# Performance work log

Hardware: AMD Instinct MI355X
Metric: run time of the kernel (lower is better)

Reference implementation:

```python
import jax, jax.numpy as jnp
from jax import lax
import numpy as np

D_IN = 512    # inputdim
HID = 128     # hiddendim
D_INNER = 2 * HID   # 256
D_PROJ = 2 * D_INNER  # 512
N_STATE = 16
R_DT = 8      # ceil(128/16)
B, H, W = 8, 32, 32


def _layernorm(y, g, b):
    mu = y.mean(-1, keepdims=True)
    var = ((y - mu) ** 2).mean(-1, keepdims=True)
    return (y - mu) / jnp.sqrt(var + 1e-5) * g + b


def _ssm(x, xw, dtw, dtb, Al, Dv, g, be):
    # x: [B, D, L] -> y: [B, L, D]  (Mamba selective scan, delta_softplus=True)
    Bb, D, L = x.shape
    n = Al.shape[1]
    xd = jnp.einsum('bdl,kd->blk', x, xw)             # [B,L,R+2N]
    dts = xd[..., :R_DT]
    Bs = xd[..., R_DT:R_DT + n]                        # [B,L,N]
    Cs = xd[..., R_DT + n:]                            # [B,L,N]
    delta = jax.nn.softplus(jnp.einsum('blr,dr->bld', dts, dtw) + dtb)  # [B,L,D]
    A = -jnp.exp(Al)                                   # [D,N]
    xt = x.transpose(0, 2, 1)                          # [B,L,D]
    dA = jnp.exp(delta[..., None] * A)                 # [B,L,D,N]
    dBx = delta[..., None] * Bs[:, :, None, :] * xt[..., None]  # [B,L,D,N]

    def step(h, inp):
        da, dbx, c = inp
        h = h * da + dbx
        return h, jnp.einsum('bdn,bn->bd', h, c)

    h0 = jnp.zeros((Bb, D, n), x.dtype)
    _, ys = lax.scan(step, h0, (dA.transpose(1, 0, 2, 3),
                                dBx.transpose(1, 0, 2, 3),
                                Cs.transpose(1, 0, 2)))
    y = ys.transpose(1, 0, 2) + xt * Dv                # [B,L,D]
    return _layernorm(y, g, be)


def _up2(y, h, w):
    Bb, L, C = y.shape
    img = y.transpose(0, 2, 1).reshape(Bb, C, h, w)
    img = jnp.repeat(jnp.repeat(img, 2, axis=2), 2, axis=3)
    return img.reshape(Bb, C, 4 * L).transpose(0, 2, 1)


def _conv1x1(x, w, b):
    return jnp.einsum('bchw,oc->bohw', x, w) + b[None, :, None, None]


def _conv2s2(x, w, b):
    out = lax.conv_general_dilated(x, w, (2, 2), 'VALID',
                                   dimension_numbers=('NCHW', 'OIHW', 'NCHW'))
    return out + b[None, :, None, None]


def _forward(input_f, in_w, in_b, c1_w, c1_b, c2_w, c2_b, c3_w, c3_b, out_w, out_b,
             xw1, dtw1, dtb1, Al1, Dv1, g1, be1,
             xw2, dtw2, dtb2, Al2, Dv2, g2, be2,
             xw3, dtw3, dtb3, Al3, Dv3, g3, be3):
    xz = _conv1x1(input_f, in_w, in_b)
    x, z = jnp.split(xz, 2, axis=1)
    f1 = _conv1x1(x, c1_w, c1_b)                      # [B,256,H,W]
    f2 = _conv2s2(f1, c2_w, c2_b)                     # [B,256,H/2,W/2]
    f3 = _conv2s2(f2, c3_w, c3_b)                     # [B,256,H/4,W/4]

    Bb, C, h3, w3 = f3.shape
    fx3 = f3.reshape(Bb, C, h3 * w3)
    y3 = _ssm(fx3, xw3, dtw3, dtb3, Al3, Dv3, g3, be3) + \
         jnp.flip(_ssm(jnp.flip(fx3, -1), xw3, dtw3, dtb3, Al3, Dv3, g3, be3), 1)
    y2_ = _up2(y3, h3, w3)

    _, _, h2, w2 = f2.shape
    fx2 = f2.reshape(Bb, C, h2 * w2)
    y2 = _ssm(fx2, xw2, dtw2, dtb2, Al2, Dv2, g2, be2) + \
         jnp.flip(_ssm(jnp.flip(fx2, -1), xw2, dtw2, dtb2, Al2, Dv2, g2, be2), 1) + y2_
    y1_ = _up2(y2, h2, w2)

    _, _, h1, w1 = f1.shape
    fx1 = f1.reshape(Bb, C, h1 * w1)
    # NOTE: source uses fssm1 forward and fssm2 on the flipped sequence
    y1 = _ssm(fx1, xw1, dtw1, dtb1, Al1, Dv1, g1, be1) + \
         jnp.flip(_ssm(jnp.flip(fx1, -1), xw2, dtw2, dtb2, Al2, Dv2, g2, be2), 1) + y1_

    out1 = y1.transpose(0, 2, 1).reshape(Bb, C, h1, w1)
    out = out1 * jax.nn.silu(z)
    return _conv1x1(out, out_w, out_b)


def setup_inputs() -> dict:
    key = jax.random.key(0)
    ks = iter(jax.random.split(key, 64))
    def nrm(shape, s=0.05):
        return (jax.random.normal(next(ks), shape, dtype=jnp.float32) * s)
    inp = {
        'input_f': jax.random.normal(next(ks), (B, D_IN, H, W), dtype=jnp.float32),
        'in_w': nrm((D_PROJ, D_IN)), 'in_b': nrm((D_PROJ,)),
        'c1_w': nrm((D_INNER, D_INNER)), 'c1_b': nrm((D_INNER,)),
        'c2_w': nrm((D_INNER, D_INNER, 2, 2)), 'c2_b': nrm((D_INNER,)),
        'c3_w': nrm((D_INNER, D_INNER, 2, 2)), 'c3_b': nrm((D_INNER,)),
        'out_w': nrm((D_IN, D_INNER)), 'out_b': nrm((D_IN,)),
    }
    Al = jnp.log(jnp.tile(jnp.arange(1, N_STATE + 1, dtype=jnp.float32), (D_INNER, 1)))
    for i in (1, 2, 3):
        inp[f'xw{i}'] = nrm((R_DT + 2 * N_STATE, D_INNER))
        inp[f'dtw{i}'] = nrm((D_INNER, R_DT), s=R_DT ** -0.5)
        inp[f'dtb{i}'] = nrm((D_INNER,)) - 4.0   # inv-softplus of small dt
        inp[f'Al{i}'] = Al
        inp[f'Dv{i}'] = jnp.ones((D_INNER,), jnp.float32)
        inp[f'g{i}'] = jnp.ones((D_INNER,), jnp.float32)
        inp[f'be{i}'] = jnp.zeros((D_INNER,), jnp.float32)
    return inp


def reference(input_f, in_w, in_b, c1_w, c1_b, c2_w, c2_b, c3_w, c3_b, out_w, out_b,
              xw1, dtw1, dtb1, Al1, Dv1, g1, be1,
              xw2, dtw2, dtb2, Al2, Dv2, g2, be2,
              xw3, dtw3, dtb3, Al3, Dv3, g3, be3):
    return _forward(input_f, in_w, in_b, c1_w, c1_b, c2_w, c2_b, c3_w, c3_b, out_w, out_b,
                    xw1, dtw1, dtb1, Al1, Dv1, g1, be1,
                    xw2, dtw2, dtb2, Al2, Dv2, g2, be2,
                    xw3, dtw3, dtb3, Al3, Dv3, g3, be3)
```

## Files before the change

### kernel.cpp

```cpp
#include <hip/hip_runtime.h>
#include <cstddef>

#define DEV static __device__ __forceinline__

typedef __attribute__((ext_vector_type(8))) short short8;
typedef __attribute__((ext_vector_type(4))) float floatx4;

DEV float siluf(float v) { return v / (1.f + expf(-v)); }

DEV unsigned short f2bf(float f) {
  unsigned int u = __float_as_uint(f);
  u += 0x7fff + ((u >> 16) & 1);
  return (unsigned short)(u >> 16);
}
DEV float bf2f(unsigned short u) {
  return __uint_as_float(((unsigned int)u) << 16);
}
DEV float4 bf2f4(ushort4 v) {
  return make_float4(bf2f(v.x), bf2f(v.y), bf2f(v.z), bf2f(v.w));
}

template <int CTRL>
DEV float qadd(float v) {
  int s = __builtin_amdgcn_update_dpp(__float_as_int(v), __float_as_int(v),
                                      CTRL, 0xF, 0xF, false);
  return v + __int_as_float(s);
}

__global__ __launch_bounds__(256) void prep_k(
    const float* __restrict__ in_w, const float* __restrict__ c1_w,
    const float* __restrict__ c2_w, const float* __restrict__ c3_w,
    const float* __restrict__ out_w, const float* __restrict__ xw1,
    const float* __restrict__ xw2, const float* __restrict__ xw3,
    unsigned short* __restrict__ wsW,
    const float* __restrict__ input_f, unsigned short* __restrict__ inT)
{
  __shared__ float tile[32][33];
  int bid = blockIdx.x;
  int t = threadIdx.x;
  if (bid < 3960) {
    int gid = bid * 256 + t;
    float v;
    if      (gid < 262144)  v = in_w[gid];
    else if (gid < 327680)  v = c1_w[gid - 262144];
    else if (gid < 589824)  {
      int off = gid - 327680;
      int o = off >> 10, kk = off & 1023, ij = kk >> 8, c = kk & 255;
      v = c2_w[o * 1024 + c * 4 + ij];
    }
    else if (gid < 851968)  {
      int off = gid - 589824;
      int o = off >> 10, kk = off & 1023, ij = kk >> 8, c = kk & 255;
      v = c3_w[o * 1024 + c * 4 + ij];
    }
    else if (gid < 983040)  v = out_w[gid - 851968];
    else if (gid < 993280)  v = xw1[gid - 983040];
    else if (gid < 1003520) v = xw2[gid - 993280];
    else                    v = xw3[gid - 1003520];
    wsW[gid] = f2bf(v);
  } else {
    int idx = bid - 3960;
    int b = idx >> 9, blk = idx & 511;
    int pt = blk & 31, ct = blk >> 5;
    int p0 = pt * 32, c0 = ct * 32;
    int r = t >> 5, cc = t & 31;
#pragma unroll
    for (int i = 0; i < 4; i++) {
      int row = r + 8 * i;
      tile[row][cc] = input_f[((size_t)b * 512 + c0 + row) * 1024 + p0 + cc];
    }
    __syncthreads();
#pragma unroll
    for (int i = 0; i < 4; i++) {
      int row = r + 8 * i;
      inT[((size_t)b * 1024 + p0 + row) * 512 + c0 + cc] = f2bf(tile[cc][row]);
    }
  }
}

template <int EPI>
DEV void mgemm_body(const unsigned short* __restrict__ A, long long sA,
                    const unsigned short* __restrict__ B, long long sB,
                    const float* __restrict__ bias,
                    void* __restrict__ O1, void* __restrict__ O2,
                    int M, int N, int K, int Mt, int Nt, int bid)
{
  __shared__ __align__(16) unsigned short Ab[128 * 40];
  __shared__ __align__(16) unsigned short Bb[128 * 40];
  int tiles = Mt * Nt;
  int bb = bid / tiles;
  int rr = bid - bb * tiles;
  int m0 = (rr / Nt) * 128;
  int n0 = (rr % Nt) * 128;
  const unsigned short* Ap = A + (size_t)bb * sA;
  const unsigned short* Bp = B + (size_t)bb * sB;

  int t = threadIdx.x;
  int lane = t & 63;
  int wm = ((t >> 7) & 1) * 64;
  int wn = ((t >> 6) & 1) * 64;
  int l15 = lane & 15, quad = lane >> 4;

  int srow = t >> 1;
  int shalf = (t & 1) * 16;
  int arow = m0 + srow; if (arow > M - 1) arow = M - 1;
  int brow = n0 + srow; if (brow > N - 1) brow = N - 1;
  const unsigned short* ap = Ap + (size_t)arow * K + shalf;
  const unsigned short* bp = Bp + (size_t)brow * K + shalf;
  unsigned short* as = &Ab[srow * 40 + shalf];
  unsigned short* bs = &Bb[srow * 40 + shalf];

  floatx4 acc[4][4] = {};

  for (int k0 = 0; k0 < K; k0 += 32) {
    uint4 a0 = *(const uint4*)(ap + k0);
    uint4 a1 = *(const uint4*)(ap + k0 + 8);
    uint4 b0 = *(const uint4*)(bp + k0);
    uint4 b1 = *(const uint4*)(bp + k0 + 8);
    __syncthreads();
    *(uint4*)as = a0; *(uint4*)(as + 8) = a1;
    *(uint4*)bs = b0; *(uint4*)(bs + 8) = b1;
    __syncthreads();
    short8 af[4], bf[4];
#pragma unroll
    for (int i = 0; i < 4; i++)
      af[i] = *(const short8*)&Ab[(wm + i * 16 + l15) * 40 + quad * 8];
#pragma unroll
    for (int j = 0; j < 4; j++)
      bf[j] = *(const short8*)&Bb[(wn + j * 16 + l15) * 40 + quad * 8];
#pragma unroll
    for (int i = 0; i < 4; i++)
#pragma unroll
      for (int j = 0; j < 4; j++)
        acc[i][j] = __builtin_amdgcn_mfma_f32_16x16x32_bf16(af[i], bf[j],
                                                            acc[i][j], 0, 0, 0);
  }

  if (EPI == 1) {
    unsigned short* Yt = (unsigned short*)O1;
    unsigned short* Ys = (unsigned short*)O2;
    float bn[4]; int nn[4];
#pragma unroll
    for (int j = 0; j < 4; j++) { nn[j] = n0 + wn + j * 16 + l15; bn[j] = bias[nn[j]]; }
#pragma unroll
    for (int i = 0; i < 4; i++) {
      int pixb = m0 + wm + i * 16 + quad * 4;
#pragma unroll
      for (int j = 0; j < 4; j++) {
        int n = nn[j];
        if (n < 256) {
#pragma unroll
          for (int r = 0; r < 4; r++)
            Yt[((size_t)bb * 1024 + pixb + r) * 256 + n] = f2bf(acc[i][j][r] + bn[j]);
        } else {
#pragma unroll
          for (int r = 0; r < 4; r++)
            Ys[((size_t)bb * 1024 + pixb + r) * 256 + (n - 256)] =
                f2bf(siluf(acc[i][j][r] + bn[j]));
        }
      }
    }
  } else {
#pragma unroll
    for (int i = 0; i < 4; i++) {
      int m = m0 + wm + i * 16 + quad * 4;
#pragma unroll
      for (int j = 0; j < 4; j++) {
        int n = n0 + wn + j * 16 + l15;
        if (m < M && n < N) {
          float vr[4];
#pragma unroll
          for (int r = 0; r < 4; r++)
            vr[r] = acc[i][j][r] + (bias ? bias[m + r] : 0.f);
          if (EPI == 0) {
            float* Y0 = (float*)O1;
            float* yp = &Y0[((size_t)bb * M + m) * N + n];
#pragma unroll
            for (int r = 0; r < 4; r++) yp[(size_t)r * N] = vr[r];
          } else {
            unsigned short* Y0b = (unsigned short*)O1;
            unsigned short* Yt  = (unsigned short*)O2;
#pragma unroll
            for (int r = 0; r < 4; r++)
              Y0b[((size_t)bb * M + m + r) * N + n] = f2bf(vr[r]);
            ushort4 o;
            o.x = f2bf(vr[0]); o.y = f2bf(vr[1]); o.z = f2bf(vr[2]); o.w = f2bf(vr[3]);
            *(ushort4*)&Yt[((size_t)bb * N + n) * M + m] = o;
          }
        }
      }
    }
  }
}

template <int EPI>
__global__ __launch_bounds__(256) void mgemm_k(
    const unsigned short* __restrict__ A, long long sA,
    const unsigned short* __restrict__ B, long long sB,
    const float* __restrict__ bias, void* __restrict__ O1, void* __restrict__ O2,
    int M, int N, int K, int Mt, int Nt)
{
  mgemm_body<EPI>(A, sA, B, sB, bias, O1, O2, M, N, K, Mt, Nt, blockIdx.x);
}

__global__ __launch_bounds__(256) void fat1_k(
    const unsigned short* __restrict__ w_xw12, const unsigned short* __restrict__ f1t,
    float* __restrict__ xd12, unsigned short* __restrict__ ic2)
{
  int bid = blockIdx.x;
  if (bid < 64) {
    mgemm_body<0>(w_xw12, 0, f1t, 1024 * 256, nullptr, xd12, nullptr,
                  80, 1024, 256, 1, 8, bid);
  } else {
    int idx = (bid - 64) * 256 + threadIdx.x;
    int cs = idx & 31, ij = (idx >> 5) & 3, n = (idx >> 7) & 255, b = idx >> 15;
    int i = ij >> 1, j = ij & 1;
    int y = n >> 4, x = n & 15;
    int pix = (2 * y + i) * 32 + 2 * x + j;
    uint4 v = *(const uint4*)&f1t[((size_t)b * 1024 + pix) * 256 + cs * 8];
    *(uint4*)&ic2[((size_t)b * 256 + n) * 1024 + ij * 256 + cs * 8] = v;
  }
}

__global__ __launch_bounds__(256) void fat2_k(
    const unsigned short* __restrict__ w_xw2, const unsigned short* __restrict__ f2t,
    float* __restrict__ xd2, unsigned short* __restrict__ ic3)
{
  int bid = blockIdx.x;
  if (bid < 16) {
    mgemm_body<0>(w_xw2, 0, f2t, 256 * 256, nullptr, xd2, nullptr,
                  40, 256, 256, 1, 2, bid);
  } else {
    int idx = (bid - 16) * 256 + threadIdx.x;
    int cs = idx & 31, ij = (idx >> 5) & 3, n = (idx >> 7) & 63, b = idx >> 13;
    int i = ij >> 1, j = ij & 1;
    int y = n >> 3, x = n & 7;
    int pix = (2 * y + i) * 16 + 2 * x + j;
    uint4 v = *(const uint4*)&f2t[((size_t)b * 256 + pix) * 256 + cs * 8];
    *(uint4*)&ic3[((size_t)b * 64 + n) * 1024 + ij * 256 + cs * 8] = v;
  }
}

__global__ __launch_bounds__(256) void post_all_k(
    const float* __restrict__ xd12, const float* __restrict__ xd2,
    const float* __restrict__ xd3,
    const float* __restrict__ dtw1, const float* __restrict__ dtb1,
    const float* __restrict__ dtw2, const float* __restrict__ dtb2,
    const float* __restrict__ dtw3, const float* __restrict__ dtb3,
    float* __restrict__ d1f, float* __restrict__ bc1f,
    float* __restrict__ d1b, float* __restrict__ bc1b,
    float* __restrict__ d2g, float* __restrict__ bc2,
    float* __restrict__ d3g, float* __restrict__ bc3)
{
  int bid = blockIdx.x;
  const float* xd; int bstride, L; const float *dtw, *dtb; float *dg, *bg;
  int lt, b;
  if (bid < 512) {
    int r = bid; lt = r & 63; b = r >> 6;
    xd = xd12; bstride = 80 * 1024; L = 1024; dtw = dtw1; dtb = dtb1; dg = d1f; bg = bc1f;
  } else if (bid < 1024) {
    int r = bid - 512; lt = r & 63; b = r >> 6;
    xd = xd12 + 40 * 1024; bstride = 80 * 1024; L = 1024; dtw = dtw2; dtb = dtb2; dg = d1b; bg = bc1b;
  } else if (bid < 1152) {
    int r = bid - 1024; lt = r & 15; b = r >> 4;
    xd = xd2; bstride = 40 * 256; L = 256; dtw = dtw2; dtb = dtb2; dg = d2g; bg = bc2;
  } else {
    int r = bid - 1152; lt = r & 3; b = r >> 2;
    xd = xd3; bstride = 40 * 64; L = 64; dtw = dtw3; dtb = dtb3; dg = d3g; bg = bc3;
  }
  int l0 = lt * 16;
  __shared__ float dl[8][16];
  int t = threadIdx.x;
  const float* xb = xd + (size_t)b * bstride + l0;
  if (t < 128) {
    int r = t >> 4, l = t & 15;
    dl[r][l] = xb[(size_t)r * L + l];
  } else {
    int tt = t - 128;
    int c = tt >> 2, seg = tt & 3;
    float4 v = *(const float4*)&xb[(size_t)(8 + c) * L + seg * 4];
    *(float4*)&bg[((size_t)b * 32 + c) * L + l0 + seg * 4] = v;
  }
  __syncthreads();
  int d = t;
  float dtwv[8];
#pragma unroll
  for (int r = 0; r < 8; r++) dtwv[r] = dtw[d * 8 + r];
  float dtbv = dtb[d];
  float spv[16];
#pragma unroll
  for (int l = 0; l < 16; l++) {
    float s = dtbv;
#pragma unroll
    for (int r = 0; r < 8; r++) s += dl[r][l] * dtwv[r];
    spv[l] = fmaxf(s, 0.f) + log1pf(expf(-fabsf(s)));
  }
  float* dout = dg + ((size_t)b * 256 + d) * L + l0;
#pragma unroll
  for (int i = 0; i < 4; i++)
    *(float4*)&dout[4 * i] = make_float4(spv[4 * i], spv[4 * i + 1],
                                         spv[4 * i + 2], spv[4 * i + 3]);
}

#define SCAN_STEPA(DVV, DXV, BVV) {                \
    float e_ = __expf((DVV) * A);                  \
    h = h * e_ + (BVV) * (DXV);                    \
    P *= e_; }

__global__ __launch_bounds__(256) void scanA_k(
    const unsigned short* __restrict__ f1b, const unsigned short* __restrict__ f2b,
    const float* __restrict__ d1f, const float* __restrict__ bc1f,
    const float* __restrict__ d1b, const float* __restrict__ bc1b,
    const float* __restrict__ d2,  const float* __restrict__ bc2,
    const float* __restrict__ Al1, const float* __restrict__ Al2,
    float* __restrict__ cP, float* __restrict__ cQ)
{
  __shared__ __align__(16) float lds[48][68];
  int bid = blockIdx.x;
  int sid, tseg, L; const unsigned short* xin; const float *dlp, *bcp, *Alp;
  if (bid < 4096) {
    sid = bid >> 4; tseg = bid & 15; L = 1024; xin = f1b;
    if (((sid >> 4) & 1) == 0) { dlp = d1f; bcp = bc1f; Alp = Al1; }
    else                       { dlp = d1b; bcp = bc1b; Alp = Al2; }
  } else {
    int idx = bid - 4096; sid = idx >> 2; tseg = idx & 3; L = 256;
    xin = f2b; dlp = d2; bcp = bc2; Alp = Al2;
  }
  int b = sid >> 5, dir = (sid >> 4) & 1, g = sid & 15;
  int t = threadIdx.x, n = t & 15, dloc = t >> 4, d = g * 16 + dloc;
  int mbase = dir ? (L - 64 * (tseg + 1)) : 64 * tseg;

  int r0 = t >> 4, cs = t & 15;
  {
    const float* p0 = dlp + ((size_t)b * 256 + g * 16 + r0) * L + mbase;
    const unsigned short* p1 = xin + ((size_t)b * 256 + g * 16 + r0) * L + mbase;
    const float* p2 = bcp + ((size_t)b * 32 + r0) * L + mbase;
    float4 v0 = *(const float4*)(p0 + cs * 4);
    float4 xf = bf2f4(*(const ushort4*)(p1 + cs * 4));
    float4 v2 = *(const float4*)(p2 + cs * 4);
    float4 dx = make_float4(v0.x * xf.x, v0.y * xf.y, v0.z * xf.z, v0.w * xf.w);
    *(float4*)&lds[r0][cs * 4]      = v0;
    *(float4*)&lds[16 + r0][cs * 4] = dx;
    *(float4*)&lds[32 + r0][cs * 4] = v2;
  }
  __syncthreads();

  float A = -expf(Alp[d * 16 + n]);
  float h = 0.f, P = 1.f;
  if (dir == 0) {
#pragma unroll
    for (int g4 = 0; g4 < 16; g4++) {
      int cb = 4 * g4;
      float4 dv4 = *(const float4*)&lds[dloc][cb];
      float4 dx4 = *(const float4*)&lds[16 + dloc][cb];
      float4 bv4 = *(const float4*)&lds[32 + n][cb];
      SCAN_STEPA(dv4.x, dx4.x, bv4.x);
      SCAN_STEPA(dv4.y, dx4.y, bv4.y);
      SCAN_STEPA(dv4.z, dx4.z, bv4.z);
      SCAN_STEPA(dv4.w, dx4.w, bv4.w);
    }
  } else {
#pragma unroll
    for (int g4 = 0; g4 < 16; g4++) {
      int cb = 60 - 4 * g4;
      float4 dv4 = *(const float4*)&lds[dloc][cb];
      float4 dx4 = *(const float4*)&lds[16 + dloc][cb];
      float4 bv4 = *(const float4*)&lds[32 + n][cb];
      SCAN_STEPA(dv4.w, dx4.w, bv4.w);
      SCAN_STEPA(dv4.z, dx4.z, bv4.z);
      SCAN_STEPA(dv4.y, dx4.y, bv4.y);
      SCAN_STEPA(dv4.x, dx4.x, bv4.x);
    }
  }
  cP[(size_t)bid * 256 + t] = P;
  cQ[(size_t)bid * 256 + t] = h;
}

#define QSTEP(DS, XU, CI, II) {                                         \
    float4 bv = *(const float4*)&ld_b[CI][n0];                          \
    float4 cv = *(const float4*)&ld_c[CI][n0];                          \
    float xs_ = bf2f(XU) * (DS);                                        \
    float4 e_;                                                          \
    e_.x = __builtin_amdgcn_exp2f((DS) * A4.x);                         \
    e_.y = __builtin_amdgcn_exp2f((DS) * A4.y);                         \
    e_.z = __builtin_amdgcn_exp2f((DS) * A4.z);                         \
    e_.w = __builtin_amdgcn_exp2f((DS) * A4.w);                         \
    h4.x = h4.x * e_.x + bv.x * xs_;                                    \
    h4.y = h4.y * e_.y + bv.y * xs_;                                    \
    h4.z = h4.z * e_.z + bv.z * xs_;                                    \
    h4.w = h4.w * e_.w + bv.w * xs_;                                    \
    float pp_ = h4.x * cv.x + h4.y * cv.y + h4.z * cv.z + h4.w * cv.w;  \
    pp_ = qadd<0xB1>(pp_);                                              \
    pp_ = qadd<0x4E>(pp_);                                              \
    ysel = (nq == (II)) ? pp_ : ysel; }

DEV float4 pcomb(float4 P, float4 h, float4 Q) {
  return make_float4(P.x * h.x + Q.x, P.y * h.y + Q.y,
                     P.z * h.z + Q.z, P.w * h.w + Q.w);
}

__global__ __launch_bounds__(256) void scanC_k(
    const unsigned short* __restrict__ f1b, const unsigned short* __restrict__ f2b,
    const unsigned short* __restrict__ f3b,
    const float* __restrict__ d1f, const float* __restrict__ bc1f,
    const float* __restrict__ d1b, const float* __restrict__ bc1b,
    const float* __restrict__ d2,  const float* __restrict__ bc2,
    const float* __restrict__ d3,  const float* __restrict__ bc3,
    float* __restrict__ y1f, float* __restrict__ y1b,
    float* __restrict__ y2f, float* __restrict__ y2b,
    float* __restrict__ y3f, float* __restrict__ y3b,
    const float* __restrict__ Al1, const float* __restrict__ Dv1,
    const float* __restrict__ Al2, const float* __restrict__ Dv2,
    const float* __restrict__ Al3, const float* __restrict__ Dv3,
    const float* __restrict__ cP, const float* __restrict__ cQ)
{
  __shared__ __align__(16) float ld_d[64][68];
  __shared__ __align__(16) unsigned short ld_xs[64][72];
  __shared__ __align__(16) float ld_b[64][20];
  __shared__ __align__(16) float ld_c[64][20];

  int bid = blockIdx.x;
  int b, dir, g4, tseg, L, lvl;
  const unsigned short* xin; const float *dlp, *bcp, *Alp, *Dvp; float* yo;
  if (bid < 1024) {
    b = bid >> 7; dir = (bid >> 6) & 1; g4 = (bid >> 4) & 3; tseg = bid & 15;
    L = 1024; xin = f1b; lvl = 1;
    if (dir == 0) { dlp = d1f; bcp = bc1f; Alp = Al1; Dvp = Dv1; yo = y1f; }
    else          { dlp = d1b; bcp = bc1b; Alp = Al2; Dvp = Dv2; yo = y1b; }
  } else if (bid < 1280) {
    int idx = bid - 1024;
    b = idx >> 5; dir = (idx >> 4) & 1; g4 = (idx >> 2) & 3; tseg = idx & 3;
    L = 256; xin = f2b; lvl = 2;
    dlp = d2; bcp = bc2; Alp = Al2; Dvp = Dv2; yo = dir ? y2b : y2f;
  } else {
    int idx = bid - 1280;
    b = idx >> 3; dir = (idx >> 2) & 1; g4 = idx & 3; tseg = 0;
    L = 64; xin = f3b; lvl = 3;
    dlp = d3; bcp = bc3; Alp = Al3; Dvp = Dv3; yo = dir ? y3b : y3f;
  }
  int mbase = dir ? (L - 64 * (tseg + 1)) : 64 * tseg;
  int t = threadIdx.x;
  int dl = t >> 2, nq = t & 3, n0 = nq * 4;
  int d = g4 * 64 + dl;

  {
    int rr = t >> 2, q = t & 3;
    const float* dr = dlp + ((size_t)b * 256 + g4 * 64 + rr) * L + mbase;
    const unsigned short* xr = xin + ((size_t)b * 256 + g4 * 64 + rr) * L + mbase;
#pragma unroll
    for (int j = 0; j < 4; ++j) {
      int c = q * 4 + 16 * j;
      float4 dv = *(const float4*)(dr + c);
      ushort4 xu = *(const ushort4*)(xr + c);
      *(float4*)&ld_d[rr][c] = dv;
      *(ushort4*)&ld_xs[rr][c] = xu;
    }
    int nn = t >> 4, c4 = t & 15;
    const float* br = bcp + ((size_t)b * 32 + nn) * L + mbase + c4 * 4;
    const float* cr = br + (size_t)16 * L;
    float4 bv = *(const float4*)br;
    float4 cv = *(const float4*)cr;
    ld_b[c4 * 4 + 0][nn] = bv.x; ld_b[c4 * 4 + 1][nn] = bv.y;
    ld_b[c4 * 4 + 2][nn] = bv.z; ld_b[c4 * 4 + 3][nn] = bv.w;
    ld_c[c4 * 4 + 0][nn] = cv.x; ld_c[c4 * 4 + 1][nn] = cv.y;
    ld_c[c4 * 4 + 2][nn] = cv.z; ld_c[c4 * 4 + 3][nn] = cv.w;
  }

  float4 A4;
  A4.x = -expf(Alp[d * 16 + n0 + 0]) * 1.442695040888963f;
  A4.y = -expf(Alp[d * 16 + n0 + 1]) * 1.442695040888963f;
  A4.z = -expf(Alp[d * 16 + n0 + 2]) * 1.442695040888963f;
  A4.w = -expf(Alp[d * 16 + n0 + 3]) * 1.442695040888963f;
  float Dvv = Dvp[d];

  float4 h4 = make_float4(0.f, 0.f, 0.f, 0.f);
  if (tseg > 0) {
    int gold = g4 * 4 + (dl >> 4);
    int soff = (lvl == 1) ? (b * 32 + dir * 16 + gold) * 16
                          : 4096 + (b * 32 + dir * 16 + gold) * 4;
    size_t cbase = (size_t)soff * 256 + (size_t)((dl & 15) * 16 + n0);
    int s = 0;
    for (; s + 4 <= tseg; s += 4) {
      const float* p = &cP[cbase + (size_t)s * 256];
      const float* q = &cQ[cbase + (size_t)s * 256];
      float4 P0 = *(const float4*)(p);       float4 Q0 = *(const float4*)(q);
      float4 P1 = *(const float4*)(p + 256); float4 Q1 = *(const float4*)(q + 256);
      float4 P2 = *(const float4*)(p + 512); float4 Q2 = *(const float4*)(q + 512);
      float4 P3 = *(const float4*)(p + 768); float4 Q3 = *(const float4*)(q + 768);
      h4 = pcomb(P0, h4, Q0); h4 = pcomb(P1, h4, Q1);
      h4 = pcomb(P2, h4, Q2); h4 = pcomb(P3, h4, Q3);
    }
    for (; s < tseg; ++s) {
      float4 P = *(const float4*)&cP[cbase + (size_t)s * 256];
      float4 Q = *(const float4*)&cQ[cbase + (size_t)s * 256];
      h4 = pcomb(P, h4, Q);
    }
  }
  __syncthreads();

  float* ybase = yo + ((size_t)b * L + mbase) * 256 + d;
  if (dir == 0) {
#pragma unroll
    for (int p = 0; p < 4; ++p) {
      float yk[4];
#pragma unroll
      for (int j = 0; j < 4; ++j) {
        int cb = 16 * p + 4 * j;
        float4 dv4 = *(const float4*)&ld_d[dl][cb];
        ushort4 xu4 = *(const ushort4*)&ld_xs[dl][cb];
        float ysel = 0.f;
        QSTEP(dv4.x, xu4.x, cb + 0, 0);
        QSTEP(dv4.y, xu4.y, cb + 1, 1);
        QSTEP(dv4.z, xu4.z, cb + 2, 2);
        QSTEP(dv4.w, xu4.w, cb + 3, 3);
        yk[j] = ysel;
      }
#pragma unroll
      for (int j = 0; j < 4; ++j) {
        int cst = 16 * p + 4 * j + nq;
        float xv = bf2f(ld_xs[dl][cst]);
        ybase[(size_t)cst * 256] = yk[j] + xv * Dvv;
      }
    }
  } else {
#pragma unroll
    for (int p = 0; p < 4; ++p) {
      float yk[4];
#pragma unroll
      for (int j = 0; j < 4; ++j) {
        int cb = 60 - 16 * p - 4 * j;
        float4 dv4 = *(const float4*)&ld_d[dl][cb];
        ushort4 xu4 = *(const ushort4*)&ld_xs[dl][cb];
        float ysel = 0.f;
        QSTEP(dv4.w, xu4.w, cb + 3, 0);
        QSTEP(dv4.z, xu4.z, cb + 2, 1);
        QSTEP(dv4.y, xu4.y, cb + 1, 2);
        QSTEP(dv4.x, xu4.x, cb + 0, 3);
        yk[j] = ysel;
      }
#pragma unroll
      for (int j = 0; j < 4; ++j) {
        int cst = 60 - 16 * p - 4 * j + (3 - nq);
        float xv = bf2f(ld_xs[dl][cst]);
        ybase[(size_t)cst * 256] = yk[j] + xv * Dvv;
      }
    }
  }
}

template <int OUTBF>
__global__ __launch_bounds__(256) void ln_combine(
    const float* __restrict__ yf, const float* __restrict__ yb,
    const float* __restrict__ gf, const float* __restrict__ bef,
    const float* __restrict__ gb, const float* __restrict__ beb,
    const float* __restrict__ up, int Wc,
    const unsigned short* __restrict__ szb, void* __restrict__ outv,
    int L, int Wf)
{
  int bid = blockIdx.x;
  int b = bid / L;
  int l = bid - b * L;
  int d = threadIdx.x;
  size_t base = ((size_t)b * L + l) * 256 + d;
  float vf = yf[base], vb = yb[base];
  float4 s = make_float4(vf, vf * vf, vb, vb * vb);
#pragma unroll
  for (int m = 1; m < 64; m <<= 1) {
    s.x += __shfl_xor(s.x, m);
    s.y += __shfl_xor(s.y, m);
    s.z += __shfl_xor(s.z, m);
    s.w += __shfl_xor(s.w, m);
  }
  __shared__ float red[4][4];
  int w = threadIdx.x >> 6;
  if ((threadIdx.x & 63) == 0) {
    red[w][0] = s.x; red[w][1] = s.y; red[w][2] = s.z; red[w][3] = s.w;
  }
  __syncthreads();
  float s0 = red[0][0] + red[1][0] + red[2][0] + red[3][0];
  float s1 = red[0][1] + red[1][1] + red[2][1] + red[3][1];
  float s2 = red[0][2] + red[1][2] + red[2][2] + red[3][2];
  float s3 = red[0][3] + red[1][3] + red[2][3] + red[3][3];
  const float inv = 1.f / 256.f;
  float muf = s0 * inv, varf = s1 * inv - muf * muf;
  float mub = s2 * inv, varb = s3 * inv - mub * mub;
  float rf = rsqrtf(varf + 1e-5f);
  float rb = rsqrtf(varb + 1e-5f);
  float v = (vf - muf) * rf * gf[d] + bef[d] + (vb - mub) * rb * gb[d] + beb[d];
  if (up) {
    int y = l / Wf, x = l - y * Wf;
    int lc = (y >> 1) * Wc + (x >> 1);
    v += up[((size_t)b * (L >> 2) + lc) * 256 + d];
  }
  if (szb) v *= bf2f(szb[base]);
  if (OUTBF) ((unsigned short*)outv)[base] = f2bf(v);
  else       ((float*)outv)[base] = v;
}

extern "C" void kernel_launch(void* const* d_in, const int* in_sizes, int n_in,
                              void* d_out, int out_size, void* d_ws, size_t ws_size,
                              hipStream_t stream) {
  (void)in_sizes; (void)n_in; (void)out_size; (void)ws_size;
  const float* input_f = (const float*)d_in[0];
  const float* in_w  = (const float*)d_in[1];
  const float* in_b  = (const float*)d_in[2];
  const float* c1_w  = (const float*)d_in[3];
  const float* c1_b  = (const float*)d_in[4];
  const float* c2_w  = (const float*)d_in[5];
  const float* c2_b  = (const float*)d_in[6];
  const float* c3_w  = (const float*)d_in[7];
  const float* c3_b  = (const float*)d_in[8];
  const float* out_w = (const float*)d_in[9];
  const float* out_b = (const float*)d_in[10];
  const float* xw1  = (const float*)d_in[11];
  const float* dtw1 = (const float*)d_in[12];
  const float* dtb1 = (const float*)d_in[13];
  const float* Al1  = (const float*)d_in[14];
  const float* Dv1  = (const float*)d_in[15];
  const float* g1   = (const float*)d_in[16];
  const float* be1  = (const float*)d_in[17];
  const float* xw2  = (const float*)d_in[18];
  const float* dtw2 = (const float*)d_in[19];
  const float* dtb2 = (const float*)d_in[20];
  const float* Al2  = (const float*)d_in[21];
  const float* Dv2  = (const float*)d_in[22];
  const float* g2   = (const float*)d_in[23];
  const float* be2  = (const float*)d_in[24];
  const float* xw3  = (const float*)d_in[25];
  const float* dtw3 = (const float*)d_in[26];
  const float* dtb3 = (const float*)d_in[27];
  const float* Al3  = (const float*)d_in[28];
  const float* Dv3  = (const float*)d_in[29];
  const float* g3   = (const float*)d_in[30];
  const float* be3  = (const float*)d_in[31];

  float* ws = (float*)d_ws;
  constexpr size_t M1 = 2097152;
  float* d1f = ws;
  unsigned short* xt = (unsigned short*)(ws + M1);
  float* y1f = ws + M1;
  unsigned short* szb = (unsigned short*)(ws + 2 * M1);
  unsigned short* f1b = (unsigned short*)(ws + 3 * M1);
  unsigned short* G = (unsigned short*)(ws + 3 * M1) + 2097152;
  float* d1b = ws + 4 * M1;
  unsigned short* inT = (unsigned short*)(ws + 5 * M1);
  unsigned short* ic2 = inT;
  unsigned short* f1t = inT + 2097152;
  unsigned short* ic3 = f1t;
  float* y1b = ws + 5 * M1;
  size_t o = 6 * M1;
  unsigned short* f2b = (unsigned short*)(ws + o); o += 524288;
  unsigned short* f3b = (unsigned short*)(ws + o); o += 131072;
  float* bc1f = ws + o; o += 262144;
  float* bc1b = ws + o; o += 262144;
  float* d2   = ws + o; o += 524288;
  float* bc2  = ws + o; o += 65536;
  float* d3   = ws + o; o += 131072;
  float* bc3  = ws + o; o += 16384;
  float* y2f  = ws + o; o += 524288;
  float* y2b  = ws + o; o += 524288;
  float* y3f  = ws + o; o += 131072;
  float* y3b  = ws + o; o += 131072;
  float* y3c  = ws + o; o += 131072;
  float* y2c  = ws + o; o += 524288;
  float* cP   = ws + o; o += 1310720;
  float* cQ   = ws + o; o += 1310720;
  unsigned short* wsW = (unsigned short*)(ws + o); o += 506880;
  float* xd12 = cP;
  float* xd2  = cP + 655360;
  float* xd3  = cP + 737280;
  unsigned short* f2t = (unsigned short*)cQ;
  unsigned short* f3t = (unsigned short*)(cQ + 262144);
  unsigned short* w_in   = wsW;
  unsigned short* w_c1   = wsW + 262144;
  unsigned short* w_c2   = wsW + 327680;
  unsigned short* w_c3   = wsW + 589824;
  unsigned short* w_out  = wsW + 851968;
  unsigned short* w_xw12 = wsW + 983040;
  unsigned short* w_xw2  = wsW + 993280;
  unsigned short* w_xw3  = wsW + 1003520;

  dim3 blk(256);

  prep_k<<<dim3(8056), blk, 0, stream>>>(in_w, c1_w, c2_w, c3_w, out_w,
                                         xw1, xw2, xw3, wsW, input_f, inT);
  mgemm_k<1><<<dim3(256), blk, 0, stream>>>(inT, 1024 * 512, w_in, 0, in_b,
                                            xt, szb, 1024, 512, 512, 8, 4);
  mgemm_k<3><<<dim3(128), blk, 0, stream>>>(w_c1, 0, xt, 1024 * 256, c1_b,
                                            f1b, f1t, 256, 1024, 256, 2, 8);
  fat1_k<<<dim3(1088), blk, 0, stream>>>(w_xw12, f1t, xd12, ic2);
  mgemm_k<3><<<dim3(32), blk, 0, stream>>>(w_c2, 0, ic2, 256 * 1024, c2_b,
                                           f2b, f2t, 256, 256, 1024, 2, 2);
  fat2_k<<<dim3(272), blk, 0, stream>>>(w_xw2, f2t, xd2, ic3);
  mgemm_k<3><<<dim3(16), blk, 0, stream>>>(w_c3, 0, ic3, 64 * 1024, c3_b,
                                           f3b, f3t, 256, 64, 1024, 2, 1);
  mgemm_k<0><<<dim3(8), blk, 0, stream>>>(w_xw3, 0, f3t, 64 * 256, nullptr,
                                          xd3, nullptr, 40, 64, 256, 1, 1);
  post_all_k<<<dim3(1184), blk, 0, stream>>>(xd12, xd2, xd3,
                                             dtw1, dtb1, dtw2, dtb2, dtw3, dtb3,
                                             d1f, bc1f, d1b, bc1b, d2, bc2, d3, bc3);
  scanA_k<<<dim3(5120), blk, 0, stream>>>(f1b, f2b, d1f, bc1f, d1b, bc1b,
                                          d2, bc2, Al1, Al2, cP, cQ);
  scanC_k<<<dim3(1344), blk, 0, stream>>>(f1b, f2b, f3b,
                                          d1f, bc1f, d1b, bc1b, d2, bc2, d3, bc3,
                                          y1f, y1b, y2f, y2b, y3f, y3b,
                                          Al1, Dv1, Al2, Dv2, Al3, Dv3, cP, cQ);
  ln_combine<0><<<dim3(512), blk, 0, stream>>>(y3f, y3b, g3, be3, g3, be3,
                                               nullptr, 0, nullptr, y3c, 64, 8);
  ln_combine<0><<<dim3(2048), blk, 0, stream>>>(y2f, y2b, g2, be2, g2, be2,
                                                y3c, 8, nullptr, y2c, 256, 16);
  ln_combine<1><<<dim3(8192), blk, 0, stream>>>(y1f, y1b, g1, be1, g2, be2,
                                                y2c, 16, szb, G, 1024, 32);
  mgemm_k<0><<<dim3(256), blk, 0, stream>>>(w_out, 0, G, 1024 * 256, out_b,
                                            (float*)d_out, nullptr,
                                            512, 1024, 256, 4, 8);
}
```

Before: 368.1 us.

## Double-buffer GEMM LDS, add small-tile conv GEMM, vectorize layernorm, exp2 scan

New measurement: 316.6 us. -14.0%, faster.

```diff
diff --git a/kernel.cpp b/kernel.cpp
--- a/kernel.cpp
+++ b/kernel.cpp
@@ -85,8 +85,8 @@
                     void* __restrict__ O1, void* __restrict__ O2,
                     int M, int N, int K, int Mt, int Nt, int bid)
 {
-  __shared__ __align__(16) unsigned short Ab[128 * 40];
-  __shared__ __align__(16) unsigned short Bb[128 * 40];
+  __shared__ __align__(16) unsigned short Ab[2 * 128 * 40];
+  __shared__ __align__(16) unsigned short Bb[2 * 128 * 40];
   int tiles = Mt * Nt;
   int bb = bid / tiles;
   int rr = bid - bb * tiles;
@@ -112,28 +112,43 @@
 
   floatx4 acc[4][4] = {};
 
+  uint4 a0 = *(const uint4*)(ap);
+  uint4 a1 = *(const uint4*)(ap + 8);
+  uint4 b0 = *(const uint4*)(bp);
+  uint4 b1 = *(const uint4*)(bp + 8);
+  *(uint4*)as = a0; *(uint4*)(as + 8) = a1;
+  *(uint4*)bs = b0; *(uint4*)(bs + 8) = b1;
+  __syncthreads();
+  int cur = 0;
   for (int k0 = 0; k0 < K; k0 += 32) {
-    uint4 a0 = *(const uint4*)(ap + k0);
-    uint4 a1 = *(const uint4*)(ap + k0 + 8);
-    uint4 b0 = *(const uint4*)(bp + k0);
-    uint4 b1 = *(const uint4*)(bp + k0 + 8);
-    __syncthreads();
-    *(uint4*)as = a0; *(uint4*)(as + 8) = a1;
-    *(uint4*)bs = b0; *(uint4*)(bs + 8) = b1;
-    __syncthreads();
-    short8 af[4], bf[4];
+    bool last = (k0 + 32 >= K);
+    if (!last) {
+      a0 = *(const uint4*)(ap + k0 + 32);
+      a1 = *(const uint4*)(ap + k0 + 40);
+      b0 = *(const uint4*)(bp + k0 + 32);
+      b1 = *(const uint4*)(bp + k0 + 40);
+    }
+    int co = cur * 5120;
+    short8 af[4], bfr[4];
 #pragma unroll
     for (int i = 0; i < 4; i++)
-      af[i] = *(const short8*)&Ab[(wm + i * 16 + l15) * 40 + quad * 8];
+      af[i] = *(const short8*)&Ab[co + (wm + i * 16 + l15) * 40 + quad * 8];
 #pragma unroll
     for (int j = 0; j < 4; j++)
-      bf[j] = *(const short8*)&Bb[(wn + j * 16 + l15) * 40 + quad * 8];
+      bfr[j] = *(const short8*)&Bb[co + (wn + j * 16 + l15) * 40 + quad * 8];
 #pragma unroll
     for (int i = 0; i < 4; i++)
 #pragma unroll
       for (int j = 0; j < 4; j++)
-        acc[i][j] = __builtin_amdgcn_mfma_f32_16x16x32_bf16(af[i], bf[j],
+        acc[i][j] = __builtin_amdgcn_mfma_f32_16x16x32_bf16(af[i], bfr[j],
                                                             acc[i][j], 0, 0, 0);
+    if (!last) {
+      int no = 5120 - co;
+      *(uint4*)(as + no) = a0; *(uint4*)(as + no + 8) = a1;
+      *(uint4*)(bs + no) = b0; *(uint4*)(bs + no + 8) = b1;
+      __syncthreads();
+      cur ^= 1;
+    }
   }
 
   if (EPI == 1) {
@@ -201,6 +216,103 @@
     int M, int N, int K, int Mt, int Nt)
 {
   mgemm_body<EPI>(A, sA, B, sB, bias, O1, O2, M, N, K, Mt, Nt, blockIdx.x);
+}
+
+__global__ __launch_bounds__(256) void cgemm_k(
+    const unsigned short* __restrict__ A,
+    const unsigned short* __restrict__ B, long long sB,
+    const float* __restrict__ bias,
+    unsigned short* __restrict__ O1, unsigned short* __restrict__ O2,
+    int M, int N, int K, int Mt, int Nt)
+{
+  __shared__ __align__(16) unsigned short Ab[2][64 * 72];
+  __shared__ __align__(16) unsigned short Bb[2][32 * 72];
+  int bid = blockIdx.x;
+  int tiles = Mt * Nt;
+  int bb = bid / tiles;
+  int rr = bid - bb * tiles;
+  int m0 = (rr / Nt) * 64;
+  int n0 = (rr % Nt) * 32;
+  const unsigned short* Bp = B + (size_t)bb * sB;
+
+  int t = threadIdx.x, lane = t & 63;
+  int wm = ((t >> 7) & 1) * 32;
+  int wn = ((t >> 6) & 1) * 16;
+  int l15 = lane & 15, quad = lane >> 4;
+
+  int ar = t >> 2, ac = (t & 3) * 16;
+  int brc = (t >> 2) & 31, bc = (t & 3) * 16;
+  const unsigned short* apc = A + (size_t)(m0 + ar) * K + ac;
+  const unsigned short* bpc = Bp + (size_t)(n0 + brc) * K + bc;
+
+  floatx4 acc2[2] = {};
+
+  uint4 av0 = *(const uint4*)(apc);
+  uint4 av1 = *(const uint4*)(apc + 8);
+  uint4 bv0 = {}, bv1 = {};
+  if (t < 128) { bv0 = *(const uint4*)(bpc); bv1 = *(const uint4*)(bpc + 8); }
+  {
+    unsigned short* asc = &Ab[0][0] + ar * 72 + ac;
+    *(uint4*)asc = av0; *(uint4*)(asc + 8) = av1;
+    if (t < 128) {
+      unsigned short* bsc = &Bb[0][0] + brc * 72 + bc;
+      *(uint4*)bsc = bv0; *(uint4*)(bsc + 8) = bv1;
+    }
+  }
+  __syncthreads();
+  int cur = 0;
+  for (int k0 = 0; k0 < K; k0 += 64) {
+    bool last = (k0 + 64 >= K);
+    if (!last) {
+      av0 = *(const uint4*)(apc + k0 + 64);
+      av1 = *(const uint4*)(apc + k0 + 72);
+      if (t < 128) {
+        bv0 = *(const uint4*)(bpc + k0 + 64);
+        bv1 = *(const uint4*)(bpc + k0 + 72);
+      }
+    }
+    const unsigned short* Ac = &Ab[cur][0];
+    const unsigned short* Bc = &Bb[cur][0];
+    short8 afc[2][2], bfc[2];
+#pragma unroll
+    for (int i = 0; i < 2; i++)
+#pragma unroll
+      for (int kk = 0; kk < 2; kk++)
+        afc[i][kk] = *(const short8*)&Ac[(wm + i * 16 + l15) * 72 + kk * 32 + quad * 8];
+#pragma unroll
+    for (int kk = 0; kk < 2; kk++)
+      bfc[kk] = *(const short8*)&Bc[(wn + l15) * 72 + kk * 32 + quad * 8];
+#pragma unroll
+    for (int kk = 0; kk < 2; kk++) {
+      acc2[0] = __builtin_amdgcn_mfma_f32_16x16x32_bf16(afc[0][kk], bfc[kk], acc2[0], 0, 0, 0);
+      acc2[1] = __builtin_amdgcn_mfma_f32_16x16x32_bf16(afc[1][kk], bfc[kk], acc2[1], 0, 0, 0);
+    }
+    if (!last) {
+      unsigned short* asn = &Ab[cur ^ 1][0] + ar * 72 + ac;
+      *(uint4*)asn = av0; *(uint4*)(asn + 8) = av1;
+      if (t < 128) {
+        unsigned short* bsn = &Bb[cur ^ 1][0] + brc * 72 + bc;
+        *(uint4*)bsn = bv0; *(uint4*)(bsn + 8) = bv1;
+      }
+      __syncthreads();
+      cur ^= 1;
+    }
+  }
+
+#pragma unroll
+  for (int i = 0; i < 2; i++) {
+    int m = m0 + wm + i * 16 + quad * 4;
+    int n = n0 + wn + l15;
+    float vr[4];
+#pragma unroll
+    for (int r = 0; r < 4; r++) vr[r] = acc2[i][r] + bias[m + r];
+#pragma unroll
+    for (int r = 0; r < 4; r++)
+      O1[((size_t)bb * M + m + r) * N + n] = f2bf(vr[r]);
+    ushort4 o;
+    o.x = f2bf(vr[0]); o.y = f2bf(vr[1]); o.z = f2bf(vr[2]); o.w = f2bf(vr[3]);
+    *(ushort4*)&O2[((size_t)bb * N + n) * M + m] = o;
+  }
 }
 
 __global__ __launch_bounds__(256) void fat1_k(
@@ -302,10 +414,10 @@
                                          spv[4 * i + 2], spv[4 * i + 3]);
 }
 
-#define SCAN_STEPA(DVV, DXV, BVV) {                \
-    float e_ = __expf((DVV) * A);                  \
-    h = h * e_ + (BVV) * (DXV);                    \
-    P *= e_; }
+#define SCAN_STEPA(DVV, DXV, BVV) {                     \
+    float e_ = __builtin_amdgcn_exp2f((DVV) * A2);      \
+    h = h * e_ + (BVV) * (DXV);                         \
+    S += (DVV); }
 
 __global__ __launch_bounds__(256) void scanA_k(
     const unsigned short* __restrict__ f1b, const unsigned short* __restrict__ f2b,
@@ -345,8 +457,8 @@
   }
   __syncthreads();
 
-  float A = -expf(Alp[d * 16 + n]);
-  float h = 0.f, P = 1.f;
+  float A2 = -expf(Alp[d * 16 + n]) * 1.442695040888963f;
+  float h = 0.f, S = 0.f;
   if (dir == 0) {
 #pragma unroll
     for (int g4 = 0; g4 < 16; g4++) {
@@ -372,7 +484,7 @@
       SCAN_STEPA(dv4.x, dx4.x, bv4.x);
     }
   }
-  cP[(size_t)bid * 256 + t] = P;
+  cP[(size_t)bid * 256 + t] = __builtin_amdgcn_exp2f(S * A2);
   cQ[(size_t)bid * 256 + t] = h;
 }
 
@@ -555,15 +667,20 @@
     const float* __restrict__ gb, const float* __restrict__ beb,
     const float* __restrict__ up, int Wc,
     const unsigned short* __restrict__ szb, void* __restrict__ outv,
-    int L, int Wf)
-{
-  int bid = blockIdx.x;
-  int b = bid / L;
-  int l = bid - b * L;
-  int d = threadIdx.x;
-  size_t base = ((size_t)b * L + l) * 256 + d;
-  float vf = yf[base], vb = yb[base];
-  float4 s = make_float4(vf, vf * vf, vb, vb * vb);
+    int L, int Lsh, int Wfsh)
+{
+  int t = threadIdx.x;
+  int row = blockIdx.x * 4 + (t >> 6);
+  int lane = t & 63;
+  int b = row >> Lsh, l = row & (L - 1);
+  size_t base = (size_t)row * 256 + lane * 4;
+  float4 vf = *(const float4*)&yf[base];
+  float4 vb = *(const float4*)&yb[base];
+  float4 s;
+  s.x = vf.x + vf.y + vf.z + vf.w;
+  s.y = vf.x * vf.x + vf.y * vf.y + vf.z * vf.z + vf.w * vf.w;
+  s.z = vb.x + vb.y + vb.z + vb.w;
+  s.w = vb.x * vb.x + vb.y * vb.y + vb.z * vb.z + vb.w * vb.w;
 #pragma unroll
   for (int m = 1; m < 64; m <<= 1) {
     s.x += __shfl_xor(s.x, m);
@@ -571,30 +688,38 @@
     s.z += __shfl_xor(s.z, m);
     s.w += __shfl_xor(s.w, m);
   }
-  __shared__ float red[4][4];
-  int w = threadIdx.x >> 6;
-  if ((threadIdx.x & 63) == 0) {
-    red[w][0] = s.x; red[w][1] = s.y; red[w][2] = s.z; red[w][3] = s.w;
-  }
-  __syncthreads();
-  float s0 = red[0][0] + red[1][0] + red[2][0] + red[3][0];
-  float s1 = red[0][1] + red[1][1] + red[2][1] + red[3][1];
-  float s2 = red[0][2] + red[1][2] + red[2][2] + red[3][2];
-  float s3 = red[0][3] + red[1][3] + red[2][3] + red[3][3];
   const float inv = 1.f / 256.f;
-  float muf = s0 * inv, varf = s1 * inv - muf * muf;
-  float mub = s2 * inv, varb = s3 * inv - mub * mub;
+  float muf = s.x * inv, varf = s.y * inv - muf * muf;
+  float mub = s.z * inv, varb = s.w * inv - mub * mub;
   float rf = rsqrtf(varf + 1e-5f);
   float rb = rsqrtf(varb + 1e-5f);
-  float v = (vf - muf) * rf * gf[d] + bef[d] + (vb - mub) * rb * gb[d] + beb[d];
+  int dc = lane * 4;
+  float4 gfv = *(const float4*)&gf[dc];
+  float4 befv = *(const float4*)&bef[dc];
+  float4 gbv = *(const float4*)&gb[dc];
+  float4 bebv = *(const float4*)&beb[dc];
+  float4 v;
+  v.x = (vf.x - muf) * rf * gfv.x + befv.x + (vb.x - mub) * rb * gbv.x + bebv.x;
+  v.y = (vf.y - muf) * rf * gfv.y + befv.y + (vb.y - mub) * rb * gbv.y + bebv.y;
+  v.z = (vf.z - muf) * rf * gfv.z + befv.z + (vb.z - mub) * rb * gbv.z + bebv.z;
+  v.w = (vf.w - muf) * rf * gfv.w + befv.w + (vb.w - mub) * rb * gbv.w + bebv.w;
   if (up) {
-    int y = l / Wf, x = l - y * Wf;
+    int y = l >> Wfsh, x = l & ((1 << Wfsh) - 1);
     int lc = (y >> 1) * Wc + (x >> 1);
-    v += up[((size_t)b * (L >> 2) + lc) * 256 + d];
-  }
-  if (szb) v *= bf2f(szb[base]);
-  if (OUTBF) ((unsigned short*)outv)[base] = f2bf(v);
-  else       ((float*)outv)[base] = v;
+    float4 uv = *(const float4*)&up[((size_t)b * (L >> 2) + lc) * 256 + dc];
+    v.x += uv.x; v.y += uv.y; v.z += uv.z; v.w += uv.w;
+  }
+  if (szb) {
+    ushort4 su = *(const ushort4*)&szb[base];
+    v.x *= bf2f(su.x); v.y *= bf2f(su.y); v.z *= bf2f(su.z); v.w *= bf2f(su.w);
+  }
+  if (OUTBF) {
+    ushort4 o;
+    o.x = f2bf(v.x); o.y = f2bf(v.y); o.z = f2bf(v.z); o.w = f2bf(v.w);
+    *(ushort4*)&((unsigned short*)outv)[base] = o;
+  } else {
+    *(float4*)&((float*)outv)[base] = v;
+  }
 }
 
 extern "C" void kernel_launch(void* const* d_in, const int* in_sizes, int n_in,
@@ -689,11 +814,11 @@
   mgemm_k<3><<<dim3(128), blk, 0, stream>>>(w_c1, 0, xt, 1024 * 256, c1_b,
                                             f1b, f1t, 256, 1024, 256, 2, 8);
   fat1_k<<<dim3(1088), blk, 0, stream>>>(w_xw12, f1t, xd12, ic2);
-  mgemm_k<3><<<dim3(32), blk, 0, stream>>>(w_c2, 0, ic2, 256 * 1024, c2_b,
-                                           f2b, f2t, 256, 256, 1024, 2, 2);
+  cgemm_k<<<dim3(256), blk, 0, stream>>>(w_c2, ic2, 256 * 1024, c2_b,
+                                         f2b, f2t, 256, 256, 1024, 4, 8);
   fat2_k<<<dim3(272), blk, 0, stream>>>(w_xw2, f2t, xd2, ic3);
-  mgemm_k<3><<<dim3(16), blk, 0, stream>>>(w_c3, 0, ic3, 64 * 1024, c3_b,
-                                           f3b, f3t, 256, 64, 1024, 2, 1);
+  cgemm_k<<<dim3(64), blk, 0, stream>>>(w_c3, ic3, 64 * 1024, c3_b,
+                                        f3b, f3t, 256, 64, 1024, 4, 2);
   mgemm_k<0><<<dim3(8), blk, 0, stream>>>(w_xw3, 0, f3t, 64 * 256, nullptr,
                                           xd3, nullptr, 40, 64, 256, 1, 1);
   post_all_k<<<dim3(1184), blk, 0, stream>>>(xd12, xd2, xd3,
@@ -705,12 +830,12 @@
                                           d1f, bc1f, d1b, bc1b, d2, bc2, d3, bc3,
                                           y1f, y1b, y2f, y2b, y3f, y3b,
                                           Al1, Dv1, Al2, Dv2, Al3, Dv3, cP, cQ);
-  ln_combine<0><<<dim3(512), blk, 0, stream>>>(y3f, y3b, g3, be3, g3, be3,
-                                               nullptr, 0, nullptr, y3c, 64, 8);
-  ln_combine<0><<<dim3(2048), blk, 0, stream>>>(y2f, y2b, g2, be2, g2, be2,
-                                                y3c, 8, nullptr, y2c, 256, 16);
-  ln_combine<1><<<dim3(8192), blk, 0, stream>>>(y1f, y1b, g1, be1, g2, be2,
-                                                y2c, 16, szb, G, 1024, 32);
+  ln_combine<0><<<dim3(128), blk, 0, stream>>>(y3f, y3b, g3, be3, g3, be3,
+                                               nullptr, 0, nullptr, y3c, 64, 6, 3);
+  ln_combine<0><<<dim3(512), blk, 0, stream>>>(y2f, y2b, g2, be2, g2, be2,
+                                               y3c, 8, nullptr, y2c, 256, 8, 4);
+  ln_combine<1><<<dim3(2048), blk, 0, stream>>>(y1f, y1b, g1, be1, g2, be2,
+                                                y2c, 16, szb, G, 1024, 10, 5);
   mgemm_k<0><<<dim3(256), blk, 0, stream>>>(w_out, 0, G, 1024 * 256, out_b,
                                             (float*)d_out, nullptr,
                                             512, 1024, 256, 4, 8);
```
